# Kernel tuning notes

Hardware: AMD Instinct MI355X
Metric: run time of the kernel (lower is better)

The kernel has to match this reference:

```python
import jax, jax.numpy as jnp
import numpy as np
from jax import lax

TOP_K = 4
N_GROUP = 4
TOPK_GROUP = 2
ROUTED_SCALE = 2.5
NEG_INF = -1e9


def setup_inputs() -> dict:
    key = jax.random.key(0)
    ks = jax.random.split(key, 6)
    B, S, H, I, E = 2, 2048, 1024, 512, 16
    x = jax.random.normal(ks[0], (B, S, H), dtype=jnp.float32)
    router_weight = jax.random.normal(ks[1], (E, H), dtype=jnp.float32) * 0.02
    router_bias = jnp.zeros((E,), dtype=jnp.float32)
    w_gate = jax.random.normal(ks[2], (E, I, H), dtype=jnp.float32) * 0.02
    w_up = jax.random.normal(ks[3], (E, I, H), dtype=jnp.float32) * 0.02
    w_down = jax.random.normal(ks[4], (E, H, I), dtype=jnp.float32) * 0.02
    return {"x": x, "router_weight": router_weight, "router_bias": router_bias,
            "w_gate": w_gate, "w_up": w_up, "w_down": w_down}


def _route(xf, router_weight, router_bias):
    # DeepSeek-V3 sigmoid router with group-limited top-k.
    T = xf.shape[0]
    E = router_weight.shape[0]
    logits = xf @ router_weight.T                      # [T, E]
    scores = jax.nn.sigmoid(logits)                    # [T, E]
    s_choice = scores + router_bias                    # bias used only for selection
    per_group = E // N_GROUP
    sg = s_choice.reshape(T, N_GROUP, per_group)
    group_scores = lax.top_k(sg, 2)[0].sum(-1)         # [T, n_group] sum of top-2
    _, gidx = lax.top_k(group_scores, TOPK_GROUP)      # [T, topk_group]
    gmask = jnp.zeros((T, N_GROUP), dtype=bool).at[jnp.arange(T)[:, None], gidx].set(True)
    masked = jnp.where(gmask[:, :, None], sg, NEG_INF).reshape(T, E)
    _, topk_idx = lax.top_k(masked, TOP_K)             # [T, top_k]
    w = jnp.take_along_axis(scores, topk_idx, axis=1)  # original sigmoid scores
    w = w / (w.sum(-1, keepdims=True) + 1e-20) * ROUTED_SCALE
    combine = jnp.zeros((T, E), dtype=xf.dtype).at[jnp.arange(T)[:, None], topk_idx].add(w)
    return combine


def reference(x, router_weight, router_bias, w_gate, w_up, w_down):
    B, S, H = x.shape
    E = w_gate.shape[0]
    xf = x.reshape(-1, H)                              # [T, H]
    combine = _route(xf, router_weight, router_bias)   # [T, E]
    # Grouped-GEMM SwiGLU experts expressed as per-expert dense GEMMs with
    # combine-weighted accumulation (same math as sort+grouped-mm+scatter).
    out = jnp.zeros_like(xf)
    for e in range(E):
        g = xf @ w_gate[e].T                           # [T, I]
        u = xf @ w_up[e].T                             # [T, I]
        y_e = (jax.nn.silu(g) * u) @ w_down[e].T       # [T, H]
        out = out + combine[:, e:e + 1] * y_e
    return out.reshape(B, S, H)
```

## Files before the change

kernel.cpp:

```cpp
#include <hip/hip_runtime.h>
#include <stdint.h>

#define T_TOK   4096
#define H_DIM   1024
#define I_DIM   512
#define E_EXP   16
#define TOPK    4
#define NTILEMAX 144

typedef __attribute__((ext_vector_type(8))) short bf16x8;
typedef __attribute__((ext_vector_type(4))) float f32x4;
typedef __attribute__((ext_vector_type(8))) unsigned short ushort8;

__device__ __forceinline__ unsigned short f2bf(float f) {
  unsigned u = __float_as_uint(f);
  u = u + 0x7fffu + ((u >> 16) & 1u);
  return (unsigned short)(u >> 16);
}
__device__ __forceinline__ float bf2f(unsigned short s) {
  return __uint_as_float(((unsigned)s) << 16);
}

__device__ __forceinline__ unsigned cvtpk(float lo, float hi) {
  unsigned r;
  asm("v_cvt_pk_bf16_f32 %0, %1, %2" : "=v"(r) : "v"(lo), "v"(hi));
  return r;
}

__device__ __forceinline__ void gload_lds16(const void* g, void* l) {
  __builtin_amdgcn_global_load_lds(
      (const __attribute__((address_space(1))) unsigned int*)g,
      (__attribute__((address_space(3))) unsigned int*)l, 16, 0, 0);
}

__global__ __launch_bounds__(256) void logits_kernel(
    const float* __restrict__ x, const float* __restrict__ rw,
    float* __restrict__ logits, unsigned short* __restrict__ xb) {
  const int t = blockIdx.x * 4 + (threadIdx.x >> 6);
  const int lane = threadIdx.x & 63;
  const float* xr = x + (size_t)t * H_DIM;

  float4 xv[4];
#pragma unroll
  for (int i = 0; i < 4; ++i) xv[i] = ((const float4*)xr)[i * 64 + lane];

  unsigned short* xrow = xb + (size_t)t * H_DIM;
#pragma unroll
  for (int i = 0; i < 4; ++i) {
    ushort4 o;
    o.x = f2bf(xv[i].x); o.y = f2bf(xv[i].y);
    o.z = f2bf(xv[i].z); o.w = f2bf(xv[i].w);
    ((ushort4*)xrow)[i * 64 + lane] = o;
  }

#pragma unroll
  for (int g = 0; g < 4; ++g) {
    float acc[4] = {0.f, 0.f, 0.f, 0.f};
#pragma unroll
    for (int e4 = 0; e4 < 4; ++e4) {
      const float* wrow = rw + (size_t)(g * 4 + e4) * H_DIM;
#pragma unroll
      for (int i = 0; i < 4; ++i) {
        float4 wv = ((const float4*)wrow)[i * 64 + lane];
        acc[e4] = fmaf(xv[i].x, wv.x, acc[e4]);
        acc[e4] = fmaf(xv[i].y, wv.y, acc[e4]);
        acc[e4] = fmaf(xv[i].z, wv.z, acc[e4]);
        acc[e4] = fmaf(xv[i].w, wv.w, acc[e4]);
      }
    }
#pragma unroll
    for (int e4 = 0; e4 < 4; ++e4)
#pragma unroll
      for (int off = 32; off > 0; off >>= 1) acc[e4] += __shfl_down(acc[e4], off, 64);
    if (lane == 0)
      ((float4*)(logits + (size_t)t * E_EXP))[g] =
          make_float4(acc[0], acc[1], acc[2], acc[3]);
  }
}

__global__ __launch_bounds__(256) void select_kernel(
    const float* __restrict__ logits, const float* __restrict__ rb,
    int* __restrict__ tidx, float* __restrict__ tw) {
  const int t = blockIdx.x * 256 + threadIdx.x;

  float sc[E_EXP], sch[E_EXP];
#pragma unroll
  for (int e = 0; e < E_EXP; ++e) {
    sc[e] = 1.f / (1.f + expf(-logits[(size_t)t * E_EXP + e]));
    sch[e] = sc[e] + rb[e];
  }

  float gsum[4];
#pragma unroll
  for (int g = 0; g < 4; ++g) {
    float m1 = -3e38f, m2 = -3e38f;
#pragma unroll
    for (int j = 0; j < 4; ++j) {
      float v = sch[g * 4 + j];
      if (v > m1) { m2 = m1; m1 = v; } else if (v > m2) { m2 = v; }
    }
    gsum[g] = m1 + m2;
  }
  int g1 = 0;
  for (int g = 1; g < 4; ++g) if (gsum[g] > gsum[g1]) g1 = g;
  int g2 = -1;
  for (int g = 0; g < 4; ++g)
    if (g != g1 && (g2 < 0 || gsum[g] > gsum[g2])) g2 = g;

  float cand[E_EXP];
#pragma unroll
  for (int e = 0; e < E_EXP; ++e)
    cand[e] = ((e >> 2) == g1 || (e >> 2) == g2) ? sch[e] : -1e9f;

  int idx[TOPK]; float wv[TOPK]; float wsum = 0.f;
#pragma unroll
  for (int k = 0; k < TOPK; ++k) {
    int bi = 0; float bv = cand[0];
#pragma unroll
    for (int e = 1; e < E_EXP; ++e) if (cand[e] > bv) { bv = cand[e]; bi = e; }
    idx[k] = bi; cand[bi] = -3e38f;
    wv[k] = sc[bi];
    wsum += wv[k];
  }
  float scale = 2.5f / (wsum + 1e-20f);
#pragma unroll
  for (int k = 0; k < TOPK; ++k) {
    tidx[t * 4 + k] = idx[k];
    tw[t * 4 + k] = wv[k] * scale;
  }
}

__global__ __launch_bounds__(256) void count_kernel(
    const int* __restrict__ tidx, int* __restrict__ counts) {
  const int e = blockIdx.x, tid = threadIdx.x;
  const int lane = tid & 63, wv = tid >> 6;
  int local = 0;
  for (int i = tid; i < T_TOK * TOPK; i += 256) local += (tidx[i] == e);
#pragma unroll
  for (int off = 32; off > 0; off >>= 1) local += __shfl_down(local, off, 64);
  __shared__ int ws[4];
  if (lane == 0) ws[wv] = local;
  __syncthreads();
  if (tid == 0) counts[e] = ws[0] + ws[1] + ws[2] + ws[3];
}

__global__ void prefix_kernel(const int* __restrict__ counts,
                              int* __restrict__ off, int* __restrict__ toff) {
  if (threadIdx.x == 0) {
    int a = 0, tt = 0;
    for (int e = 0; e < E_EXP; ++e) {
      off[e] = a; toff[e] = tt;
      a += counts[e];
      tt += (counts[e] + 127) >> 7;
    }
    off[E_EXP] = a;
    toff[E_EXP] = tt;
  }
}

__global__ __launch_bounds__(256) void scatter_kernel(
    const int* __restrict__ tidx, const int* __restrict__ off,
    int* __restrict__ rowmap, int* __restrict__ rowtok) {
  const int e = blockIdx.x, tid = threadIdx.x;
  const int lane = tid & 63, wv = tid >> 6;
  __shared__ int wsum[4];
  __shared__ int srun;
  if (tid == 0) srun = 0;
  __syncthreads();
  const int base = off[e];
  for (int c = 0; c < T_TOK * TOPK / 256; ++c) {
    const int i = c * 256 + tid;
    const bool f = (tidx[i] == e);
    unsigned long long m = __ballot(f);
    int wpre = __popcll(m & ((1ull << lane) - 1ull));
    if (lane == 63) wsum[wv] = wpre + (f ? 1 : 0);
    __syncthreads();
    const int run = srun;
    int pre = 0, tot = 0;
#pragma unroll
    for (int w = 0; w < 4; ++w) {
      int v = wsum[w];
      if (w < wv) pre += v;
      tot += v;
    }
    if (f) {
      const int pos = base + run + pre + wpre;
      rowmap[i] = pos;
      rowtok[pos] = i >> 2;
    }
    __syncthreads();
    if (tid == 0) srun = run + tot;
  }
}

__device__ __forceinline__ int find_expert(const int* __restrict__ toff, int tile) {
  int e = 0;
#pragma unroll
  for (int q = 1; q <= E_EXP; ++q) e += (toff[q] <= tile);
  return e;
}

__global__ __launch_bounds__(256, 3) void gateup_kernel(
    const unsigned short* __restrict__ xbf,
    const float* __restrict__ wgf,
    const float* __restrict__ wuf,
    const int* __restrict__ rowtok, const int* __restrict__ off,
    const int* __restrict__ toff,
    unsigned short* __restrict__ hbuf) {
  const int bid = (int)blockIdx.x;
  const int work = (bid & 7) * NTILEMAX + (bid >> 3);
  const int tile = work >> 3, tn = work & 7;
  if (tile >= toff[E_EXP]) return;
  const int e = find_expert(toff, tile);
  const int tm = tile - toff[e];
  const int seg0 = off[e];
  const int nrows = off[e + 1] - seg0;

  __shared__ __align__(16) unsigned short As[128 * 64];
  __shared__ __align__(16) unsigned short Gs[64 * 64];
  __shared__ __align__(16) unsigned short Us[64 * 64];
  __shared__ int ids[128];

  const int tid = threadIdx.x;
  if (tid < 128) {
    int r = tm * 128 + tid;
    ids[tid] = rowtok[seg0 + (r < nrows ? r : 0)];
  }
  __syncthreads();

  const int col8 = tid & 7;
  const int r0 = tid >> 3;
  const int csrc = (col8 ^ (r0 & 7)) * 8;
  const int bcol = col8 * 8;
  const int bdst = (col8 ^ (r0 & 7)) * 8;
  int tokA[4];
#pragma unroll
  for (int j = 0; j < 4; ++j) tokA[j] = ids[j * 32 + r0];

  const float* wg = wgf + (size_t)e * I_DIM * H_DIM + (size_t)(tn * 64) * H_DIM;
  const float* wu = wuf + (size_t)e * I_DIM * H_DIM + (size_t)(tn * 64) * H_DIM;

  f32x4 accg[4][2], accu[4][2];
#pragma unroll
  for (int m = 0; m < 4; ++m)
#pragma unroll
    for (int n = 0; n < 2; ++n) { accg[m][n] = (f32x4)0.f; accu[m][n] = (f32x4)0.f; }

  const int lane = tid & 63, wid = tid >> 6;
  const int wr = wid >> 1, wc = wid & 1;
  const int frow = lane & 15, fr7 = frow & 7;
  const int kc = lane >> 4;

  for (int kt = 0; kt < H_DIM / 64; ++kt) {
    const int kbA = kt * 64 + csrc;
    const int kbB = kt * 64 + bcol;
    __syncthreads();
#pragma unroll
    for (int j = 0; j < 4; ++j)
      gload_lds16(xbf + ((size_t)tokA[j] * H_DIM + kbA), (char*)As + (j * 256 + tid) * 16);
#pragma unroll
    for (int j = 0; j < 2; ++j) {
      const int row = j * 32 + r0;
      const float4* gs = (const float4*)(wg + (size_t)row * H_DIM + kbB);
      const float4* us = (const float4*)(wu + (size_t)row * H_DIM + kbB);
      float4 g0 = gs[0], g1 = gs[1];
      float4 u0 = us[0], u1 = us[1];
      uint4 gw, uw;
      gw.x = cvtpk(g0.x, g0.y); gw.y = cvtpk(g0.z, g0.w);
      gw.z = cvtpk(g1.x, g1.y); gw.w = cvtpk(g1.z, g1.w);
      uw.x = cvtpk(u0.x, u0.y); uw.y = cvtpk(u0.z, u0.w);
      uw.z = cvtpk(u1.x, u1.y); uw.w = cvtpk(u1.z, u1.w);
      *(uint4*)&Gs[row * 64 + bdst] = gw;
      *(uint4*)&Us[row * 64 + bdst] = uw;
    }
    __syncthreads();
#pragma unroll
    for (int kk = 0; kk < 2; ++kk) {
      const int swz = ((kk * 4 + kc) ^ fr7) * 8;
      bf16x8 af[4], bg[2], bu[2];
#pragma unroll
      for (int m = 0; m < 4; ++m)
        af[m] = *(const bf16x8*)&As[(wr * 64 + m * 16 + frow) * 64 + swz];
#pragma unroll
      for (int n = 0; n < 2; ++n) {
        bg[n] = *(const bf16x8*)&Gs[(wc * 32 + n * 16 + frow) * 64 + swz];
        bu[n] = *(const bf16x8*)&Us[(wc * 32 + n * 16 + frow) * 64 + swz];
      }
#pragma unroll
      for (int m = 0; m < 4; ++m)
#pragma unroll
        for (int n = 0; n < 2; ++n) {
          accg[m][n] = __builtin_amdgcn_mfma_f32_16x16x32_bf16(af[m], bg[n], accg[m][n], 0, 0, 0);
          accu[m][n] = __builtin_amdgcn_mfma_f32_16x16x32_bf16(af[m], bu[n], accu[m][n], 0, 0, 0);
        }
    }
  }

  const int lr = (lane >> 4) * 4, lc = lane & 15;
#pragma unroll
  for (int m = 0; m < 4; ++m) {
#pragma unroll
    for (int j = 0; j < 4; ++j) {
      int r = tm * 128 + wr * 64 + m * 16 + lr + j;
      if (r < nrows) {
        size_t rowoff = (size_t)(seg0 + r) * I_DIM;
#pragma unroll
        for (int n = 0; n < 2; ++n) {
          float g = accg[m][n][j];
          float u = accu[m][n][j];
          float hv = g / (1.f + __expf(-g)) * u;
          hbuf[rowoff + tn * 64 + wc * 32 + n * 16 + lc] = f2bf(hv);
        }
      }
    }
  }
}

__global__ __launch_bounds__(256, 3) void down_kernel(
    const unsigned short* __restrict__ hbuf,
    const float* __restrict__ wdf,
    const int* __restrict__ off, const int* __restrict__ toff,
    unsigned short* __restrict__ ybuf) {
  const int bid = (int)blockIdx.x;
  const int work = (bid & 7) * NTILEMAX + (bid >> 3);
  const int tile = work >> 3, tn = work & 7;
  if (tile >= toff[E_EXP]) return;
  const int e = find_expert(toff, tile);
  const int tm = tile - toff[e];
  const int seg0 = off[e];
  const int nrows = off[e + 1] - seg0;

  __shared__ __align__(16) unsigned short As[128 * 64];
  __shared__ __align__(16) unsigned short Bs[128 * 64];

  const int tid = threadIdx.x;
  const int col8 = tid & 7;
  const int r0 = tid >> 3;
  const int csrc = (col8 ^ (r0 & 7)) * 8;
  const int bcol = col8 * 8;
  const int bdst = (col8 ^ (r0 & 7)) * 8;
  int rowA[4];
#pragma unroll
  for (int j = 0; j < 4; ++j) {
    int r = tm * 128 + j * 32 + r0;
    rowA[j] = seg0 + (r < nrows ? r : nrows - 1);
  }
  const float* wd = wdf + (size_t)e * H_DIM * I_DIM + (size_t)(tn * 128) * I_DIM;

  f32x4 acc[4][4];
#pragma unroll
  for (int m = 0; m < 4; ++m)
#pragma unroll
    for (int n = 0; n < 4; ++n) acc[m][n] = (f32x4)0.f;

  const int lane = tid & 63, wid = tid >> 6;
  const int wr = wid >> 1, wc = wid & 1;
  const int frow = lane & 15, fr7 = frow & 7;
  const int kc = lane >> 4;

  for (int kt = 0; kt < I_DIM / 64; ++kt) {
    const int kbA = kt * 64 + csrc;
    const int kbB = kt * 64 + bcol;
    __syncthreads();
#pragma unroll
    for (int j = 0; j < 4; ++j)
      gload_lds16(hbuf + ((size_t)rowA[j] * I_DIM + kbA), (char*)As + (j * 256 + tid) * 16);
#pragma unroll
    for (int j = 0; j < 4; ++j) {
      const int row = j * 32 + r0;
      const float4* ds = (const float4*)(wd + (size_t)row * I_DIM + kbB);
      float4 d0 = ds[0], d1 = ds[1];
      uint4 w;
      w.x = cvtpk(d0.x, d0.y); w.y = cvtpk(d0.z, d0.w);
      w.z = cvtpk(d1.x, d1.y); w.w = cvtpk(d1.z, d1.w);
      *(uint4*)&Bs[row * 64 + bdst] = w;
    }
    __syncthreads();
#pragma unroll
    for (int kk = 0; kk < 2; ++kk) {
      const int swz = ((kk * 4 + kc) ^ fr7) * 8;
      bf16x8 af[4], bw[4];
#pragma unroll
      for (int m = 0; m < 4; ++m)
        af[m] = *(const bf16x8*)&As[(wr * 64 + m * 16 + frow) * 64 + swz];
#pragma unroll
      for (int n = 0; n < 4; ++n)
        bw[n] = *(const bf16x8*)&Bs[(wc * 64 + n * 16 + frow) * 64 + swz];
#pragma unroll
      for (int m = 0; m < 4; ++m)
#pragma unroll
        for (int n = 0; n < 4; ++n)
          acc[m][n] = __builtin_amdgcn_mfma_f32_16x16x32_bf16(af[m], bw[n], acc[m][n], 0, 0, 0);
    }
  }

  const int lr = (lane >> 4) * 4, lc = lane & 15;
#pragma unroll
  for (int m = 0; m < 4; ++m) {
#pragma unroll
    for (int j = 0; j < 4; ++j) {
      int r = tm * 128 + wr * 64 + m * 16 + lr + j;
      if (r < nrows) {
        size_t rowoff = (size_t)(seg0 + r) * H_DIM;
#pragma unroll
        for (int n = 0; n < 4; ++n)
          ybuf[rowoff + tn * 128 + wc * 64 + n * 16 + lc] = f2bf(acc[m][n][j]);
      }
    }
  }
}

__global__ __launch_bounds__(256) void combine_kernel(
    const unsigned short* __restrict__ ybuf, const int* __restrict__ rowmap,
    const float* __restrict__ tw, float* __restrict__ out) {
  int t = blockIdx.x, tid = threadIdx.x;
  __shared__ int rloc[4];
  __shared__ float wloc[4];
  if (tid < 4) { rloc[tid] = rowmap[t * 4 + tid]; wloc[tid] = tw[t * 4 + tid]; }
  __syncthreads();
  int c = tid * 4;
  float4 a = {0.f, 0.f, 0.f, 0.f};
#pragma unroll
  for (int k = 0; k < 4; ++k) {
    ushort4 v = *(const ushort4*)&ybuf[(size_t)rloc[k] * H_DIM + c];
    float w = wloc[k];
    a.x += w * bf2f(v.x); a.y += w * bf2f(v.y);
    a.z += w * bf2f(v.z); a.w += w * bf2f(v.w);
  }
  *(float4*)&out[(size_t)t * H_DIM + c] = a;
}

extern "C" void kernel_launch(void* const* d_in, const int* in_sizes, int n_in,
                              void* d_out, int out_size, void* d_ws, size_t ws_size,
                              hipStream_t stream) {
  (void)in_sizes; (void)n_in; (void)out_size; (void)ws_size;
  const float* x  = (const float*)d_in[0];
  const float* rw = (const float*)d_in[1];
  const float* rb = (const float*)d_in[2];
  const float* wg = (const float*)d_in[3];
  const float* wu = (const float*)d_in[4];
  const float* wd = (const float*)d_in[5];
  float* out = (float*)d_out;

  char* base = (char*)d_ws;
  size_t o = 0;
  auto alloc = [&](size_t b) -> void* {
    void* p = base + o;
    o += (b + 255) & ~(size_t)255;
    return p;
  };
  unsigned short* xbf   = (unsigned short*)alloc((size_t)T_TOK * H_DIM * 2);
  unsigned short* hbuf  = (unsigned short*)alloc((size_t)T_TOK * TOPK * I_DIM * 2);
  unsigned short* ybuf  = (unsigned short*)alloc((size_t)T_TOK * TOPK * H_DIM * 2);
  float* logits = (float*)alloc((size_t)T_TOK * E_EXP * 4);
  int*   tidx   = (int*)alloc((size_t)T_TOK * TOPK * 4);
  float* tw     = (float*)alloc((size_t)T_TOK * TOPK * 4);
  int*   rowmap = (int*)alloc((size_t)T_TOK * TOPK * 4);
  int*   rowtok = (int*)alloc((size_t)T_TOK * TOPK * 4);
  int*   counts = (int*)alloc(256);
  int*   offb   = (int*)alloc(256);
  int*   toffb  = (int*)alloc(256);

  logits_kernel<<<T_TOK / 4, 256, 0, stream>>>(x, rw, logits, xbf);
  select_kernel<<<T_TOK / 256, 256, 0, stream>>>(logits, rb, tidx, tw);
  count_kernel<<<E_EXP, 256, 0, stream>>>(tidx, counts);
  prefix_kernel<<<1, 64, 0, stream>>>(counts, offb, toffb);
  scatter_kernel<<<E_EXP, 256, 0, stream>>>(tidx, offb, rowmap, rowtok);

  gateup_kernel<<<8 * NTILEMAX, 256, 0, stream>>>(xbf, wg, wu, rowtok, offb, toffb, hbuf);
  down_kernel<<<8 * NTILEMAX, 256, 0, stream>>>(hbuf, wd, offb, toffb, ybuf);
  combine_kernel<<<T_TOK, 256, 0, stream>>>(ybuf, rowmap, tw, out);
}
```

Before: 156.4 us.

## Register-prefetch next fp32 weight tile during MFMA in expert GEMMs

Both expert GEMM kernels (gate/up and down) now load the next k-tile's fp32 weights into registers before the MFMA loop of the current tile. This overlaps global weight-load latency with compute instead of stalling at the start of each iteration. Sched barriers keep the loads issued ahead of the MFMAs, and the leading __syncthreads is replaced by a raw s_barrier at the loop end. The cost is higher register pressure from the prefetch buffers. There is also a risk that the async LDS loads for A are not fully waited on, because s_barrier alone does not wait for outstanding memory.

```diff
diff --git a/kernel.cpp b/kernel.cpp
--- a/kernel.cpp
+++ b/kernel.cpp
@@ -10,7 +10,6 @@
 
 typedef __attribute__((ext_vector_type(8))) short bf16x8;
 typedef __attribute__((ext_vector_type(4))) float f32x4;
-typedef __attribute__((ext_vector_type(8))) unsigned short ushort8;
 
 __device__ __forceinline__ unsigned short f2bf(float f) {
   unsigned u = __float_as_uint(f);
@@ -251,29 +250,39 @@
   const int frow = lane & 15, fr7 = frow & 7;
   const int kc = lane >> 4;
 
-  for (int kt = 0; kt < H_DIM / 64; ++kt) {
+  const int NT = H_DIM / 64;
+  float4 Bg[2][2], Bu[2][2];
+
+  auto loadB = [&](int kt) {
+#pragma unroll
+    for (int j = 0; j < 2; ++j) {
+      const float* gs = wg + (size_t)(j * 32 + r0) * H_DIM + kt * 64 + bcol;
+      const float* us = wu + (size_t)(j * 32 + r0) * H_DIM + kt * 64 + bcol;
+      Bg[j][0] = ((const float4*)gs)[0]; Bg[j][1] = ((const float4*)gs)[1];
+      Bu[j][0] = ((const float4*)us)[0]; Bu[j][1] = ((const float4*)us)[1];
+    }
+  };
+
+  loadB(0);
+  for (int kt = 0; kt < NT; ++kt) {
     const int kbA = kt * 64 + csrc;
-    const int kbB = kt * 64 + bcol;
-    __syncthreads();
 #pragma unroll
     for (int j = 0; j < 4; ++j)
       gload_lds16(xbf + ((size_t)tokA[j] * H_DIM + kbA), (char*)As + (j * 256 + tid) * 16);
 #pragma unroll
     for (int j = 0; j < 2; ++j) {
       const int row = j * 32 + r0;
-      const float4* gs = (const float4*)(wg + (size_t)row * H_DIM + kbB);
-      const float4* us = (const float4*)(wu + (size_t)row * H_DIM + kbB);
-      float4 g0 = gs[0], g1 = gs[1];
-      float4 u0 = us[0], u1 = us[1];
       uint4 gw, uw;
-      gw.x = cvtpk(g0.x, g0.y); gw.y = cvtpk(g0.z, g0.w);
-      gw.z = cvtpk(g1.x, g1.y); gw.w = cvtpk(g1.z, g1.w);
-      uw.x = cvtpk(u0.x, u0.y); uw.y = cvtpk(u0.z, u0.w);
-      uw.z = cvtpk(u1.x, u1.y); uw.w = cvtpk(u1.z, u1.w);
+      gw.x = cvtpk(Bg[j][0].x, Bg[j][0].y); gw.y = cvtpk(Bg[j][0].z, Bg[j][0].w);
+      gw.z = cvtpk(Bg[j][1].x, Bg[j][1].y); gw.w = cvtpk(Bg[j][1].z, Bg[j][1].w);
+      uw.x = cvtpk(Bu[j][0].x, Bu[j][0].y); uw.y = cvtpk(Bu[j][0].z, Bu[j][0].w);
+      uw.z = cvtpk(Bu[j][1].x, Bu[j][1].y); uw.w = cvtpk(Bu[j][1].z, Bu[j][1].w);
       *(uint4*)&Gs[row * 64 + bdst] = gw;
       *(uint4*)&Us[row * 64 + bdst] = uw;
     }
     __syncthreads();
+    if (kt + 1 < NT) loadB(kt + 1);
+    __builtin_amdgcn_sched_barrier(0);
 #pragma unroll
     for (int kk = 0; kk < 2; ++kk) {
       const int swz = ((kk * 4 + kc) ^ fr7) * 8;
@@ -294,6 +303,9 @@
           accu[m][n] = __builtin_amdgcn_mfma_f32_16x16x32_bf16(af[m], bu[n], accu[m][n], 0, 0, 0);
         }
     }
+    __builtin_amdgcn_sched_barrier(0);
+    __builtin_amdgcn_s_barrier();
+    __builtin_amdgcn_sched_barrier(0);
   }
 
   const int lr = (lane >> 4) * 4, lc = lane & 15;
@@ -358,24 +370,34 @@
   const int frow = lane & 15, fr7 = frow & 7;
   const int kc = lane >> 4;
 
-  for (int kt = 0; kt < I_DIM / 64; ++kt) {
+  const int NT = I_DIM / 64;
+  float4 Bd[4][2];
+
+  auto loadB = [&](int kt) {
+#pragma unroll
+    for (int j = 0; j < 4; ++j) {
+      const float* ds = wd + (size_t)(j * 32 + r0) * I_DIM + kt * 64 + bcol;
+      Bd[j][0] = ((const float4*)ds)[0]; Bd[j][1] = ((const float4*)ds)[1];
+    }
+  };
+
+  loadB(0);
+  for (int kt = 0; kt < NT; ++kt) {
     const int kbA = kt * 64 + csrc;
-    const int kbB = kt * 64 + bcol;
-    __syncthreads();
 #pragma unroll
     for (int j = 0; j < 4; ++j)
       gload_lds16(hbuf + ((size_t)rowA[j] * I_DIM + kbA), (char*)As + (j * 256 + tid) * 16);
 #pragma unroll
     for (int j = 0; j < 4; ++j) {
       const int row = j * 32 + r0;
-      const float4* ds = (const float4*)(wd + (size_t)row * I_DIM + kbB);
-      float4 d0 = ds[0], d1 = ds[1];
       uint4 w;
-      w.x = cvtpk(d0.x, d0.y); w.y = cvtpk(d0.z, d0.w);
-      w.z = cvtpk(d1.x, d1.y); w.w = cvtpk(d1.z, d1.w);
+      w.x = cvtpk(Bd[j][0].x, Bd[j][0].y); w.y = cvtpk(Bd[j][0].z, Bd[j][0].w);
+      w.z = cvtpk(Bd[j][1].x, Bd[j][1].y); w.w = cvtpk(Bd[j][1].z, Bd[j][1].w);
       *(uint4*)&Bs[row * 64 + bdst] = w;
     }
     __syncthreads();
+    if (kt + 1 < NT) loadB(kt + 1);
+    __builtin_amdgcn_sched_barrier(0);
 #pragma unroll
     for (int kk = 0; kk < 2; ++kk) {
       const int swz = ((kk * 4 + kc) ^ fr7) * 8;
@@ -392,6 +414,9 @@
         for (int n = 0; n < 4; ++n)
           acc[m][n] = __builtin_amdgcn_mfma_f32_16x16x32_bf16(af[m], bw[n], acc[m][n], 0, 0, 0);
     }
+    __builtin_amdgcn_sched_barrier(0);
+    __builtin_amdgcn_s_barrier();
+    __builtin_amdgcn_sched_barrier(0);
   }
 
   const int lr = (lane >> 4) * 4, lc = lane & 15;
```

Result: faster. 151.6 us (-3.0%).
